# Kernel tuning notes

Measured on AMD Instinct MI355X. Metric: run time of the kernel, lower is better.

Reference implementation:

```python
import jax, jax.numpy as jnp
import numpy as np

D, NH, NL, NP, DFF = 256, 8, 4, 4, 1024
DH = D // NH
# 4-level FPN of a 1024x1024 image at strides 8/16/32/64 (H, W per level)
SHAPES = np.array([[128, 128], [64, 64], [32, 32], [16, 16]], dtype=np.int32)


def setup_inputs() -> dict:
    ks = jax.random.split(jax.random.key(0), 16)
    B, Lq = 4, 900
    sizes = SHAPES[:, 0] * SHAPES[:, 1]
    Lin = int(sizes.sum())
    starts = np.concatenate([[0], np.cumsum(sizes)[:-1]]).astype(np.int32)
    s = 0.02  # small init so softmax/LN stay well-conditioned

    def w(k, shape):
        return jax.random.normal(k, shape, jnp.float32) * s

    return {
        "tgt": jax.random.normal(ks[0], (Lq, B, D), jnp.float32),
        "tgt_reference_points": jax.random.uniform(ks[1], (Lq, B, NL, 2), jnp.float32),
        "memory": jax.random.normal(ks[2], (Lin, B, D), jnp.float32),
        "W_off": w(ks[3], (NH * NL * NP * 2, D)), "b_off": w(ks[4], (NH * NL * NP * 2,)),
        "W_attn": w(ks[5], (NH * NL * NP, D)), "b_attn": w(ks[6], (NH * NL * NP,)),
        "W_val": w(ks[7], (D, D)), "b_val": w(ks[8], (D,)),
        "W_out": w(ks[9], (D, D)), "b_out": w(ks[10], (D,)),
        "ln1_g": jnp.ones((D,), jnp.float32), "ln1_b": jnp.zeros((D,), jnp.float32),
        "W1": w(ks[11], (DFF, D)), "b1": w(ks[12], (DFF,)),
        "W2": w(ks[13], (D, DFF)), "b2": w(ks[14], (D,)),
        "ln3_g": jnp.ones((D,), jnp.float32), "ln3_b": jnp.zeros((D,), jnp.float32),
        "memory_spatial_shapes": jnp.asarray(SHAPES),
        "memory_level_start_index": jnp.asarray(starts),
        "memory_key_padding_mask": jnp.zeros((B, Lin), jnp.bool_),
    }


def _ln(x, g, b, eps=1e-5):
    mu = x.mean(-1, keepdims=True)
    var = ((x - mu) ** 2).mean(-1, keepdims=True)
    return (x - mu) * jax.lax.rsqrt(var + eps) * g + b


def _bilinear(vl, loc, H, W):
    # vl: (B, NH, H*W, DH); loc: (B, Lq, NH, NP, 2) normalized to [0,1]
    # matches torch grid_sample(mode='bilinear', padding_mode='zeros', align_corners=False)
    B, Lq, nh, P, _ = loc.shape
    x = loc[..., 0] * W - 0.5
    y = loc[..., 1] * H - 0.5
    x0f = jnp.floor(x)
    y0f = jnp.floor(y)
    x0 = x0f.astype(jnp.int32)
    y0 = y0f.astype(jnp.int32)
    wx1 = x - x0f
    wy1 = y - y0f

    def tap(xi, yi, w):
        valid = (xi >= 0) & (xi < W) & (yi >= 0) & (yi < H)
        idx = jnp.clip(yi, 0, H - 1) * W + jnp.clip(xi, 0, W - 1)
        idx = idx.transpose(0, 2, 1, 3).reshape(B, nh, Lq * P)
        ww = (w * valid).transpose(0, 2, 1, 3).reshape(B, nh, Lq * P)
        vals = jnp.take_along_axis(vl, idx[..., None], axis=2)  # (B,NH,Lq*P,DH)
        return vals * ww[..., None]

    acc = (tap(x0, y0, (1 - wx1) * (1 - wy1)) + tap(x0 + 1, y0, wx1 * (1 - wy1))
           + tap(x0, y0 + 1, (1 - wx1) * wy1) + tap(x0 + 1, y0 + 1, wx1 * wy1))
    return acc.reshape(B, nh, Lq, P, DH)


def _msda(q, ref, value, shapes_np, W_off, b_off, W_attn, b_attn, W_out, b_out):
    # q: (B,Lq,D), ref: (B,Lq,NL,2), value: (B,Lin,NH,DH)
    B, Lq, _ = q.shape
    off = (q @ W_off.T + b_off).reshape(B, Lq, NH, NL, NP, 2)
    a = jax.nn.softmax((q @ W_attn.T + b_attn).reshape(B, Lq, NH, NL * NP), axis=-1)
    a = a.reshape(B, Lq, NH, NL, NP)
    norm = jnp.asarray(shapes_np[:, ::-1].copy(), jnp.float32)  # (NL, 2) as (W, H)
    loc = ref[:, :, None, :, None, :] + off / norm[None, None, None, :, None, :]
    sizes = [int(h) * int(w) for h, w in shapes_np]
    starts = np.concatenate([[0], np.cumsum(sizes)[:-1]])
    v = value.transpose(0, 2, 1, 3)  # (B, NH, Lin, DH)
    out = jnp.zeros((B, NH, Lq, DH), q.dtype)
    for l, (H, W) in enumerate(shapes_np):
        vl = v[:, :, int(starts[l]):int(starts[l]) + sizes[l], :]
        sampled = _bilinear(vl, loc[:, :, :, l], int(H), int(W))  # (B,NH,Lq,NP,DH)
        wl = a[:, :, :, l].transpose(0, 2, 1, 3)  # (B,NH,Lq,NP)
        out = out + (sampled * wl[..., None]).sum(3)
    out = out.transpose(0, 2, 1, 3).reshape(B, Lq, D)
    return out @ W_out.T + b_out


def reference(tgt, tgt_reference_points, memory, W_off, b_off, W_attn, b_attn,
              W_val, b_val, W_out, b_out, ln1_g, ln1_b, W1, b1, W2, b2, ln3_g, ln3_b,
              memory_spatial_shapes, memory_level_start_index, memory_key_padding_mask):
    shapes_np = np.asarray(memory_spatial_shapes)  # static level metadata
    q = tgt.transpose(1, 0, 2)                      # (B, Lq, D)
    ref = tgt_reference_points.transpose(1, 0, 2, 3)
    mem = memory.transpose(1, 0, 2)                 # (B, Lin, D)
    B, Lin, _ = mem.shape
    value = mem @ W_val.T + b_val
    value = jnp.where(memory_key_padding_mask[..., None], 0.0, value)
    value = value.reshape(B, Lin, NH, DH)
    ca = _msda(q, ref, value, shapes_np, W_off, b_off, W_attn, b_attn, W_out, b_out)
    # residual + LN (dropout is identity in eval)
    t = _ln(tgt + ca.transpose(1, 0, 2), ln1_g, ln1_b)
    # FFN
    t2 = jax.nn.relu(t @ W1.T + b1) @ W2.T + b2
    return _ln(t + t2, ln3_g, ln3_b)
```

## Files before the change

### kernel.cpp

```cpp
#include <hip/hip_runtime.h>
#include <hip/hip_bf16.h>

#define B_   4
#define LQ_  900
#define D_   256
#define NH_  8
#define DH_  32
#define NL_  4
#define NP_  4
#define DFF_ 1024
#define LIN_ 21760
#define MQ_  (LQ_*B_)
#define MV_  (LIN_*B_)

typedef __attribute__((ext_vector_type(8))) short bh8;
typedef __attribute__((ext_vector_type(4))) float f32x4;

__device__ __forceinline__ short bf16b(float f) {
    __hip_bfloat16 h = __float2bfloat16(f);
    return *reinterpret_cast<short*>(&h);
}

__device__ __forceinline__ void gload_lds16(const void* g, void* l) {
    __builtin_amdgcn_global_load_lds(
        (const __attribute__((address_space(1))) unsigned int*)g,
        (__attribute__((address_space(3))) unsigned int*)l, 16, 0, 0);
}

__device__ __forceinline__ bh8 af_from_f32(const float* p) {
    float4 v0 = *reinterpret_cast<const float4*>(p);
    float4 v1 = *reinterpret_cast<const float4*>(p + 4);
    return (bh8){ bf16b(v0.x), bf16b(v0.y), bf16b(v0.z), bf16b(v0.w),
                  bf16b(v1.x), bf16b(v1.y), bf16b(v1.z), bf16b(v1.w) };
}

__global__ __launch_bounds__(256)
void wprep_k(const float* __restrict__ Woff, const float* __restrict__ Wattn,
             const float* __restrict__ Wout, const float* __restrict__ W1,
             const float* __restrict__ W2, const float* __restrict__ Wval,
             unsigned char* __restrict__ qkvimg, unsigned char* __restrict__ outimg,
             unsigned char* __restrict__ w1img, unsigned char* __restrict__ w2img,
             unsigned char* __restrict__ valimg)
{
    const int cid = blockIdx.x*256 + threadIdx.x;
    const float* W; unsigned char* img; int KQ, c;
    if      (cid < 8192)  { W=Woff;  img=qkvimg;           KQ=8;  c=cid;       }
    else if (cid < 12288) { W=Wattn; img=qkvimg + 131072;  KQ=8;  c=cid-8192;  }
    else if (cid < 20480) { W=Wout;  img=outimg;           KQ=8;  c=cid-12288; }
    else if (cid < 53248) { W=W1;    img=w1img;            KQ=8;  c=cid-20480; }
    else if (cid < 86016) { W=W2;    img=w2img;            KQ=32; c=cid-53248; }
    else                  { W=Wval;  img=valimg;           KQ=8;  c=cid-86016; }
    const int K   = KQ*32;
    const int n16 = c & 15, g = (c>>4)&3, t = c>>6;
    const int kq  = t & (KQ-1);
    const int ntile = t >> ((KQ==8) ? 3 : 5);
    const int n = ntile*16 + n16, k0 = kq*32 + g*8;
    float4 v0 = *reinterpret_cast<const float4*>(&W[(size_t)n*K + k0]);
    float4 v1 = *reinterpret_cast<const float4*>(&W[(size_t)n*K + k0 + 4]);
    union { short s[8]; uint4 u; } pk;
    pk.s[0]=bf16b(v0.x); pk.s[1]=bf16b(v0.y); pk.s[2]=bf16b(v0.z); pk.s[3]=bf16b(v0.w);
    pk.s[4]=bf16b(v1.x); pk.s[5]=bf16b(v1.y); pk.s[6]=bf16b(v1.z); pk.s[7]=bf16b(v1.w);
    *reinterpret_cast<uint4*>(img + (size_t)(ntile*KQ + kq)*1024 + (g*16+n16)*16) = pk.u;
}

__global__ __launch_bounds__(256, 4)
void val_gemm_k(const float* __restrict__ A, const unsigned char* __restrict__ Wimg,
                const float* __restrict__ bias, unsigned short* __restrict__ C,
                const unsigned char* __restrict__ mask)
{
    __shared__ __align__(16) unsigned char Al[32768];

    const int tid  = threadIdx.x;
    const int lane = tid & 63;
    const int wc   = tid >> 6;
    const int m0   = blockIdx.x * 32;
    const int r16  = lane & 15;
    const int g    = lane >> 4;

    const unsigned char* Abyte = (const unsigned char*)A;
    const unsigned char* wlane = Wimg + lane*16;

    const int a_row = (tid >> 3) & 31;
    const int a_x   = (tid & 7) * 16;
    const size_t a_src_row = (size_t)(m0 + a_row) * 1024 + (a_x ^ ((a_row & 7) << 4));
    const int a_dst = tid * 16;

#define ISSUE_A(KQ) gload_lds16(Abyte + a_src_row + (KQ)*128, (char*)Al + (KQ)*4096 + a_dst)
#define ISSUE_W(KQ, SLOT)                                                              \
    do { _Pragma("unroll")                                                             \
        for (int i_ = 0; i_ < 4; ++i_)                                                 \
            bfr[SLOT][i_] = *reinterpret_cast<const bh8*>(                             \
                wlane + (size_t)((wc*4 + i_)*8 + (KQ))*1024);                          \
    } while (0)

    bh8 bfr[3][4];

    ISSUE_A(0);
    ISSUE_W(0, 0);
    ISSUE_W(1, 1);
    ISSUE_A(1);
    ISSUE_A(2);

    f32x4 acc[2][4];
    #pragma unroll
    for (int i = 0; i < 2; ++i)
        #pragma unroll
        for (int j = 0; j < 4; ++j) acc[i][j] = (f32x4){0.f,0.f,0.f,0.f};

    #pragma unroll
    for (int kq = 0; kq < 8; ++kq) {
        if (kq < 6)      asm volatile("s_waitcnt vmcnt(6)" ::: "memory");
        else if (kq == 6) asm volatile("s_waitcnt vmcnt(5)" ::: "memory");
        else              asm volatile("s_waitcnt vmcnt(0)" ::: "memory");
        __builtin_amdgcn_s_barrier();

        bh8 af[2];
        #pragma unroll
        for (int mf = 0; mf < 2; ++mf) {
            const int row = mf*16 + r16;
            const int swz = (row & 7) << 4;
            const char* base = (const char*)Al + kq*4096 + row*128;
            float4 v0 = *reinterpret_cast<const float4*>(base + ((g*32     ) ^ swz));
            float4 v1 = *reinterpret_cast<const float4*>(base + ((g*32 + 16) ^ swz));
            af[mf] = (bh8){ bf16b(v0.x), bf16b(v0.y), bf16b(v0.z), bf16b(v0.w),
                            bf16b(v1.x), bf16b(v1.y), bf16b(v1.z), bf16b(v1.w) };
        }

        if (kq == 0) { ISSUE_W(2, 2); ISSUE_A(3); }
        if (kq == 1) { ISSUE_W(3, 0); ISSUE_A(4); }
        if (kq == 2) { ISSUE_W(4, 1); ISSUE_A(5); }
        if (kq == 3) { ISSUE_W(5, 2); ISSUE_A(6); }
        if (kq == 4) { ISSUE_W(6, 0); ISSUE_A(7); }
        if (kq == 5) { ISSUE_W(7, 1); }

        #pragma unroll
        for (int mf = 0; mf < 2; ++mf)
            #pragma unroll
            for (int i = 0; i < 4; ++i)
                acc[mf][i] = __builtin_amdgcn_mfma_f32_16x16x32_bf16(af[mf], bfr[kq % 3][i], acc[mf][i], 0, 0, 0);
    }
#undef ISSUE_A
#undef ISSUE_W

    float bv[4];
    #pragma unroll
    for (int i = 0; i < 4; ++i) bv[i] = bias[wc*64 + i*16 + r16];

    #pragma unroll
    for (int mf = 0; mf < 2; ++mf) {
        #pragma unroll
        for (int r = 0; r < 4; ++r) {
            const int gm = m0 + mf*16 + g*4 + r;
            const bool z = mask[(gm & 3)*LIN_ + (gm >> 2)] != 0;
            #pragma unroll
            for (int i = 0; i < 4; ++i) {
                float v = acc[mf][i][r] + bv[i];
                if (z) v = 0.f;
                C[(size_t)gm*256 + wc*64 + i*16 + r16] = (unsigned short)bf16b(v);
            }
        }
    }
}

__global__ __launch_bounds__(512)
void qkv_k(const float* __restrict__ A, const unsigned char* __restrict__ Wimg,
           const float* __restrict__ b_off, const float* __restrict__ b_attn,
           float* __restrict__ Yoff, float* __restrict__ Yattn)
{
    const int tid = threadIdx.x, lane = tid & 63, w = tid >> 6;
    const int m16 = lane & 15, g = lane >> 4;
    const int m0 = blockIdx.x * 16;

    bh8 af[8];
    #pragma unroll
    for (int kq = 0; kq < 8; ++kq)
        af[kq] = af_from_f32(&A[(size_t)(m0 + m16)*256 + kq*32 + g*8]);

    f32x4 acc[3];
    #pragma unroll
    for (int i = 0; i < 3; ++i) acc[i] = (f32x4){0.f,0.f,0.f,0.f};

    #pragma unroll
    for (int i = 0; i < 3; ++i) {
        const int nt = w*3 + i;
        #pragma unroll
        for (int kq = 0; kq < 8; ++kq) {
            bh8 bf = *reinterpret_cast<const bh8*>(Wimg + (size_t)(nt*8 + kq)*1024 + lane*16);
            acc[i] = __builtin_amdgcn_mfma_f32_16x16x32_bf16(af[kq], bf, acc[i], 0, 0, 0);
        }
    }

    #pragma unroll
    for (int i = 0; i < 3; ++i) {
        const int nt = w*3 + i;
        const int j  = nt*16 + m16;
        #pragma unroll
        for (int r = 0; r < 4; ++r) {
            const int m = m0 + g*4 + r;
            if (nt < 16) Yoff[(size_t)m*256 + j] = acc[i][r] + b_off[j];
            else         Yattn[(size_t)m*128 + (j-256)] = acc[i][r] + b_attn[j-256];
        }
    }
}

__global__ __launch_bounds__(1024, 4)
void outln_k(const float* __restrict__ A, const unsigned char* __restrict__ Wimg,
             const float* __restrict__ bias, const float* __restrict__ res,
             const float* __restrict__ lg, const float* __restrict__ lb,
             float* __restrict__ T)
{
    __shared__ float sln[16][256];

    const int tid = threadIdx.x, lane = tid & 63, w = tid >> 6;
    const int m16 = lane & 15, g = lane >> 4;
    const int m0 = blockIdx.x * 16;

    bh8 af[8];
    #pragma unroll
    for (int kq = 0; kq < 8; ++kq)
        af[kq] = af_from_f32(&A[(size_t)(m0 + m16)*256 + kq*32 + g*8]);

    f32x4 acc = (f32x4){0.f,0.f,0.f,0.f};
    #pragma unroll
    for (int kq = 0; kq < 8; ++kq) {
        bh8 bf = *reinterpret_cast<const bh8*>(Wimg + (size_t)(w*8 + kq)*1024 + lane*16);
        acc = __builtin_amdgcn_mfma_f32_16x16x32_bf16(af[kq], bf, acc, 0, 0, 0);
    }

    const int j = w*16 + m16;
    #pragma unroll
    for (int r = 0; r < 4; ++r) {
        const int ml = g*4 + r;
        sln[ml][j] = acc[r] + bias[j] + res[(size_t)(m0 + ml)*256 + j];
    }
    __syncthreads();

    const int row = tid >> 6, l2 = tid & 63;
    float v[4], s1 = 0.f, s2 = 0.f;
    #pragma unroll
    for (int c = 0; c < 4; ++c) {
        v[c] = sln[row][l2 + c*64];
        s1 += v[c]; s2 += v[c]*v[c];
    }
    #pragma unroll
    for (int o = 32; o >= 1; o >>= 1) {
        s1 += __shfl_xor(s1, o, 64);
        s2 += __shfl_xor(s2, o, 64);
    }
    const float mu  = s1 * (1.f/256.f);
    const float var = s2 * (1.f/256.f) - mu*mu;
    const float is  = rsqrtf(var + 1e-5f);
    #pragma unroll
    for (int c = 0; c < 4; ++c) {
        const int jj = l2 + c*64;
        T[(size_t)(m0 + row)*256 + jj] = (v[c] - mu) * is * lg[jj] + lb[jj];
    }
}

__global__ __launch_bounds__(1024, 4)
void ffnln_k(const float* __restrict__ T, const unsigned char* __restrict__ W1img,
             const float* __restrict__ b1, const unsigned char* __restrict__ W2img,
             const float* __restrict__ b2, const float* __restrict__ lg,
             const float* __restrict__ lb, float* __restrict__ Yout)
{
    __shared__ __align__(16) short hl[2][16*272];
    __shared__ float sln[16][256];

    const int tid = threadIdx.x, lane = tid & 63, w = tid >> 6;
    const int m16 = lane & 15, g = lane >> 4;
    const int m0 = blockIdx.x * 16;

    bh8 af1[8];
    #pragma unroll
    for (int kq = 0; kq < 8; ++kq)
        af1[kq] = af_from_f32(&T[(size_t)(m0 + m16)*256 + kq*32 + g*8]);

    f32x4 yacc = (f32x4){0.f,0.f,0.f,0.f};

    int buf = 0;
    #pragma unroll
    for (int fc = 0; fc < 4; ++fc) {
        const int ftile_g = fc*16 + w;
        f32x4 hacc = (f32x4){0.f,0.f,0.f,0.f};
        #pragma unroll
        for (int kq = 0; kq < 8; ++kq) {
            bh8 bf = *reinterpret_cast<const bh8*>(W1img + (size_t)(ftile_g*8 + kq)*1024 + lane*16);
            hacc = __builtin_amdgcn_mfma_f32_16x16x32_bf16(af1[kq], bf, hacc, 0, 0, 0);
        }
        const float bb = b1[ftile_g*16 + m16];
        #pragma unroll
        for (int r = 0; r < 4; ++r) {
            const float v = fmaxf(hacc[r] + bb, 0.f);
            hl[buf][(g*4 + r)*272 + w*16 + m16] = bf16b(v);
        }
        __syncthreads();
        bh8 a2[8];
        #pragma unroll
        for (int kqf = 0; kqf < 8; ++kqf)
            a2[kqf] = *reinterpret_cast<const bh8*>((const char*)&hl[buf][0]
                + m16*544 + (kqf*32 + g*8)*2);
        #pragma unroll
        for (int kqf = 0; kqf < 8; ++kqf) {
            const int kq2 = fc*8 + kqf;
            bh8 bf = *reinterpret_cast<const bh8*>(W2img + (size_t)(w*32 + kq2)*1024 + lane*16);
            yacc = __builtin_amdgcn_mfma_f32_16x16x32_bf16(a2[kqf], bf, yacc, 0, 0, 0);
        }
        buf ^= 1;
    }

    const int j = w*16 + m16;
    #pragma unroll
    for (int r = 0; r < 4; ++r) {
        const int ml = g*4 + r;
        sln[ml][j] = yacc[r] + b2[j] + T[(size_t)(m0 + ml)*256 + j];
    }
    __syncthreads();

    const int row = tid >> 6, l2 = tid & 63;
    float v[4], s1 = 0.f, s2 = 0.f;
    #pragma unroll
    for (int c = 0; c < 4; ++c) {
        v[c] = sln[row][l2 + c*64];
        s1 += v[c]; s2 += v[c]*v[c];
    }
    #pragma unroll
    for (int o = 32; o >= 1; o >>= 1) {
        s1 += __shfl_xor(s1, o, 64);
        s2 += __shfl_xor(s2, o, 64);
    }
    const float mu  = s1 * (1.f/256.f);
    const float var = s2 * (1.f/256.f) - mu*mu;
    const float is  = rsqrtf(var + 1e-5f);
    #pragma unroll
    for (int c = 0; c < 4; ++c) {
        const int jj = l2 + c*64;
        Yout[(size_t)(m0 + row)*256 + jj] = (v[c] - mu) * is * lg[jj] + lb[jj];
    }
}

__global__ __launch_bounds__(256)
void msda_k(const float* __restrict__ off,
            const float* __restrict__ attnlog,
            const float* __restrict__ refp,
            const __hip_bfloat16* __restrict__ value,
            float* __restrict__ out)
{
    const int m = blockIdx.x;
    const int b = m & 3;
    const int d = threadIdx.x;
    const int h = d >> 5;

    __shared__ float s_off[256];
    __shared__ float s_al[128];
    __shared__ float s_ref[NL_*2];
    s_off[d] = off[(size_t)m*256 + d];
    if (d < 128) s_al[d] = attnlog[(size_t)m*128 + d];
    if (d < NL_*2) s_ref[d] = refp[(size_t)m*(NL_*2) + d];
    __syncthreads();

    float mx = -1e30f;
    #pragma unroll
    for (int t = 0; t < 16; ++t) mx = fmaxf(mx, s_al[h*16 + t]);
    float e[16], ssum = 0.f;
    #pragma unroll
    for (int t = 0; t < 16; ++t) { e[t] = __expf(s_al[h*16 + t] - mx); ssum += e[t]; }
    const float inv = 1.f / ssum;

    const int HS[4] = {128, 64, 32, 16};
    const int ST[4] = {0, 16384, 20480, 21504};

    float acc = 0.f;
    #pragma unroll
    for (int l = 0; l < NL_; ++l) {
        const int H = HS[l], W = HS[l], st = ST[l];
        const float rx = s_ref[l*2+0], ry = s_ref[l*2+1];
        #pragma unroll
        for (int p = 0; p < NP_; ++p) {
            const int base = ((h*NL_ + l)*NP_ + p);
            const float a  = e[l*4 + p] * inv;
            const float ox = s_off[base*2+0], oy = s_off[base*2+1];
            const float x = rx*(float)W + ox - 0.5f;
            const float y = ry*(float)H + oy - 0.5f;
            const float x0f = floorf(x), y0f = floorf(y);
            const int x0 = (int)x0f, y0 = (int)y0f;
            const float wx1 = x - x0f, wy1 = y - y0f;
            const float wx0 = 1.f - wx1, wy0 = 1.f - wy1;
            #pragma unroll
            for (int t = 0; t < 4; ++t) {
                const int xi = x0 + (t & 1);
                const int yi = y0 + (t >> 1);
                const float wgt = (t==0 ? wx0*wy0 : t==1 ? wx1*wy0 : t==2 ? wx0*wy1 : wx1*wy1);
                if (xi >= 0 && xi < W && yi >= 0 && yi < H) {
                    const size_t idx = (size_t)(st + yi*W + xi);
                    const float v = __bfloat162float(value[(idx*B_ + b)*D_ + d]);
                    acc = fmaf(a*wgt, v, acc);
                }
            }
        }
    }
    out[(size_t)m*256 + d] = acc;
}

extern "C" void kernel_launch(void* const* d_in, const int* in_sizes, int n_in,
                              void* d_out, int out_size, void* d_ws, size_t ws_size,
                              hipStream_t stream)
{
    const float* tgt    = (const float*)d_in[0];
    const float* refp   = (const float*)d_in[1];
    const float* mem    = (const float*)d_in[2];
    const float* W_off  = (const float*)d_in[3];
    const float* b_off  = (const float*)d_in[4];
    const float* W_attn = (const float*)d_in[5];
    const float* b_attn = (const float*)d_in[6];
    const float* W_val  = (const float*)d_in[7];
    const float* b_val  = (const float*)d_in[8];
    const float* W_out  = (const float*)d_in[9];
    const float* b_out  = (const float*)d_in[10];
    const float* ln1g   = (const float*)d_in[11];
    const float* ln1b   = (const float*)d_in[12];
    const float* W1     = (const float*)d_in[13];
    const float* b1     = (const float*)d_in[14];
    const float* W2     = (const float*)d_in[15];
    const float* b2     = (const float*)d_in[16];
    const float* ln3g   = (const float*)d_in[17];
    const float* ln3b   = (const float*)d_in[18];
    const unsigned char* mask = (const unsigned char*)d_in[21];
    float* out = (float*)d_out;

    char* p = (char*)d_ws;
    __hip_bfloat16* value = (__hip_bfloat16*)p; p += (size_t)MV_*D_*2;
    float* offb = (float*)p; p += (size_t)MQ_*256*4;
    float* attl = (float*)p; p += (size_t)MQ_*128*4;
    float* msda = (float*)p; p += (size_t)MQ_*256*4;
    float* tb   = (float*)p; p += (size_t)MQ_*256*4;
    unsigned char* qkvimg = (unsigned char*)p; p += 196608;
    unsigned char* outimg = (unsigned char*)p; p += 131072;
    unsigned char* w1img  = (unsigned char*)p; p += 524288;
    unsigned char* w2img  = (unsigned char*)p; p += 524288;
    unsigned char* valimg = (unsigned char*)p; p += 131072;
    (void)ws_size; (void)in_sizes; (void)n_in; (void)out_size;

    wprep_k<<<dim3(368), dim3(256), 0, stream>>>(W_off, W_attn, W_out, W1, W2, W_val,
                                                 qkvimg, outimg, w1img, w2img, valimg);
    val_gemm_k<<<dim3(MV_/32), dim3(256), 0, stream>>>(mem, valimg, b_val,
                                                       (unsigned short*)value, mask);
    qkv_k<<<dim3(MQ_/16), dim3(512), 0, stream>>>(tgt, qkvimg, b_off, b_attn, offb, attl);
    msda_k<<<dim3(MQ_), dim3(256), 0, stream>>>(offb, attl, refp, value, msda);
    outln_k<<<dim3(MQ_/16), dim3(1024), 0, stream>>>(msda, outimg, b_out, tgt, ln1g, ln1b, tb);
    ffnln_k<<<dim3(MQ_/16), dim3(1024), 0, stream>>>(tb, w1img, b1, w2img, b2, ln3g, ln3b, out);
}
```

Before: 118.2 us.

## Split value GEMM N across two blocks with a 4-slot LDS ring

The value-projection GEMM now launches twice as many blocks, each computing half of the 256 output columns for a 32-row tile. The A-tile LDS staging drops from 8 slots to a 4-slot ring, halving shared memory, and the launch bound rises to 8 blocks per CU. The 3-deep register prefetch of B fragments is replaced by per-iteration loads of fewer fragments. The aim is more occupancy and parallelism, at the cost of reading each fp32 A tile twice (relying on L2) and exposing B-load latency directly.

```diff
diff --git a/kernel.cpp b/kernel.cpp
--- a/kernel.cpp
+++ b/kernel.cpp
@@ -63,19 +63,21 @@
     *reinterpret_cast<uint4*>(img + (size_t)(ntile*KQ + kq)*1024 + (g*16+n16)*16) = pk.u;
 }
 
-__global__ __launch_bounds__(256, 4)
+__global__ __launch_bounds__(256, 8)
 void val_gemm_k(const float* __restrict__ A, const unsigned char* __restrict__ Wimg,
                 const float* __restrict__ bias, unsigned short* __restrict__ C,
                 const unsigned char* __restrict__ mask)
 {
-    __shared__ __align__(16) unsigned char Al[32768];
-
-    const int tid  = threadIdx.x;
-    const int lane = tid & 63;
-    const int wc   = tid >> 6;
-    const int m0   = blockIdx.x * 32;
-    const int r16  = lane & 15;
-    const int g    = lane >> 4;
+    __shared__ __align__(16) unsigned char Al[16384];
+
+    const int tid   = threadIdx.x;
+    const int lane  = tid & 63;
+    const int wc    = tid >> 6;
+    const int mt    = blockIdx.x >> 1;
+    const int nhalf = blockIdx.x & 1;
+    const int m0    = mt * 32;
+    const int r16   = lane & 15;
+    const int g     = lane >> 4;
 
     const unsigned char* Abyte = (const unsigned char*)A;
     const unsigned char* wlane = Wimg + lane*16;
@@ -85,32 +87,22 @@
     const size_t a_src_row = (size_t)(m0 + a_row) * 1024 + (a_x ^ ((a_row & 7) << 4));
     const int a_dst = tid * 16;
 
-#define ISSUE_A(KQ) gload_lds16(Abyte + a_src_row + (KQ)*128, (char*)Al + (KQ)*4096 + a_dst)
-#define ISSUE_W(KQ, SLOT)                                                              \
-    do { _Pragma("unroll")                                                             \
-        for (int i_ = 0; i_ < 4; ++i_)                                                 \
-            bfr[SLOT][i_] = *reinterpret_cast<const bh8*>(                             \
-                wlane + (size_t)((wc*4 + i_)*8 + (KQ))*1024);                          \
-    } while (0)
-
-    bh8 bfr[3][4];
+#define ISSUE_A(KQ) gload_lds16(Abyte + a_src_row + (KQ)*128, (char*)Al + ((KQ)&3)*4096 + a_dst)
 
     ISSUE_A(0);
-    ISSUE_W(0, 0);
-    ISSUE_W(1, 1);
     ISSUE_A(1);
     ISSUE_A(2);
 
-    f32x4 acc[2][4];
+    f32x4 acc[2][2];
     #pragma unroll
     for (int i = 0; i < 2; ++i)
         #pragma unroll
-        for (int j = 0; j < 4; ++j) acc[i][j] = (f32x4){0.f,0.f,0.f,0.f};
+        for (int j = 0; j < 2; ++j) acc[i][j] = (f32x4){0.f,0.f,0.f,0.f};
 
     #pragma unroll
     for (int kq = 0; kq < 8; ++kq) {
-        if (kq < 6)      asm volatile("s_waitcnt vmcnt(6)" ::: "memory");
-        else if (kq == 6) asm volatile("s_waitcnt vmcnt(5)" ::: "memory");
+        if (kq < 6)      asm volatile("s_waitcnt vmcnt(2)" ::: "memory");
+        else if (kq == 6) asm volatile("s_waitcnt vmcnt(1)" ::: "memory");
         else              asm volatile("s_waitcnt vmcnt(0)" ::: "memory");
         __builtin_amdgcn_s_barrier();
 
@@ -119,32 +111,29 @@
         for (int mf = 0; mf < 2; ++mf) {
             const int row = mf*16 + r16;
             const int swz = (row & 7) << 4;
-            const char* base = (const char*)Al + kq*4096 + row*128;
+            const char* base = (const char*)Al + (kq & 3)*4096 + row*128;
             float4 v0 = *reinterpret_cast<const float4*>(base + ((g*32     ) ^ swz));
             float4 v1 = *reinterpret_cast<const float4*>(base + ((g*32 + 16) ^ swz));
             af[mf] = (bh8){ bf16b(v0.x), bf16b(v0.y), bf16b(v0.z), bf16b(v0.w),
                             bf16b(v1.x), bf16b(v1.y), bf16b(v1.z), bf16b(v1.w) };
         }
 
-        if (kq == 0) { ISSUE_W(2, 2); ISSUE_A(3); }
-        if (kq == 1) { ISSUE_W(3, 0); ISSUE_A(4); }
-        if (kq == 2) { ISSUE_W(4, 1); ISSUE_A(5); }
-        if (kq == 3) { ISSUE_W(5, 2); ISSUE_A(6); }
-        if (kq == 4) { ISSUE_W(6, 0); ISSUE_A(7); }
-        if (kq == 5) { ISSUE_W(7, 1); }
-
-        #pragma unroll
-        for (int mf = 0; mf < 2; ++mf)
+        if (kq < 5) ISSUE_A(kq + 3);
+
+        #pragma unroll
+        for (int i = 0; i < 2; ++i) {
+            const int nt = nhalf*8 + wc*2 + i;
+            bh8 bf = *reinterpret_cast<const bh8*>(wlane + (size_t)(nt*8 + kq)*1024);
             #pragma unroll
-            for (int i = 0; i < 4; ++i)
-                acc[mf][i] = __builtin_amdgcn_mfma_f32_16x16x32_bf16(af[mf], bfr[kq % 3][i], acc[mf][i], 0, 0, 0);
+            for (int mf = 0; mf < 2; ++mf)
+                acc[mf][i] = __builtin_amdgcn_mfma_f32_16x16x32_bf16(af[mf], bf, acc[mf][i], 0, 0, 0);
+        }
     }
 #undef ISSUE_A
-#undef ISSUE_W
-
-    float bv[4];
-    #pragma unroll
-    for (int i = 0; i < 4; ++i) bv[i] = bias[wc*64 + i*16 + r16];
+
+    float bv[2];
+    #pragma unroll
+    for (int i = 0; i < 2; ++i) bv[i] = bias[nhalf*128 + wc*32 + i*16 + r16];
 
     #pragma unroll
     for (int mf = 0; mf < 2; ++mf) {
@@ -153,10 +142,10 @@
             const int gm = m0 + mf*16 + g*4 + r;
             const bool z = mask[(gm & 3)*LIN_ + (gm >> 2)] != 0;
             #pragma unroll
-            for (int i = 0; i < 4; ++i) {
+            for (int i = 0; i < 2; ++i) {
                 float v = acc[mf][i][r] + bv[i];
                 if (z) v = 0.f;
-                C[(size_t)gm*256 + wc*64 + i*16 + r16] = (unsigned short)bf16b(v);
+                C[(size_t)gm*256 + nhalf*128 + wc*32 + i*16 + r16] = (unsigned short)bf16b(v);
             }
         }
     }
@@ -442,8 +431,8 @@
 
     wprep_k<<<dim3(368), dim3(256), 0, stream>>>(W_off, W_attn, W_out, W1, W2, W_val,
                                                  qkvimg, outimg, w1img, w2img, valimg);
-    val_gemm_k<<<dim3(MV_/32), dim3(256), 0, stream>>>(mem, valimg, b_val,
-                                                       (unsigned short*)value, mask);
+    val_gemm_k<<<dim3((MV_/32)*2), dim3(256), 0, stream>>>(mem, valimg, b_val,
+                                                           (unsigned short*)value, mask);
     qkv_k<<<dim3(MQ_/16), dim3(512), 0, stream>>>(tgt, qkvimg, b_off, b_attn, offb, attl);
     msda_k<<<dim3(MQ_), dim3(256), 0, stream>>>(offb, attl, refp, value, msda);
     outln_k<<<dim3(MQ_/16), dim3(1024), 0, stream>>>(msda, outimg, b_out, tgt, ln1g, ln1b, tb);
```

Result: slower. 126.2 us (+6.8%).

## Fuse value and offset/attn projection GEMMs; fuse out-proj LN with FFN LN

Applied to the files above, without the earlier changes.

Merges the value projection GEMM and the query offset/attention projection into one launch, with the query blocks appended after the value blocks. The query part now uses 256-thread blocks, so each wave computes 6 N-tiles instead of 3. It also fuses the output projection, residual and first LayerNorm into the FFN kernel, keeping the normalized rows in shared memory. This removes the intermediate tb buffer round-trip and two kernel launches. The cost is lower occupancy on the fused FFN kernel (launch bounds 1024,2) and more register pressure in the qkv branch.

```diff
diff --git a/kernel.cpp b/kernel.cpp
--- a/kernel.cpp
+++ b/kernel.cpp
@@ -12,6 +12,7 @@
 #define LIN_ 21760
 #define MQ_  (LQ_*B_)
 #define MV_  (LIN_*B_)
+#define VALBLKS (MV_/32)
 
 typedef __attribute__((ext_vector_type(8))) short bh8;
 typedef __attribute__((ext_vector_type(4))) float f32x4;
@@ -64,26 +65,31 @@
 }
 
 __global__ __launch_bounds__(256, 4)
-void val_gemm_k(const float* __restrict__ A, const unsigned char* __restrict__ Wimg,
-                const float* __restrict__ bias, unsigned short* __restrict__ C,
-                const unsigned char* __restrict__ mask)
+void valqkv_k(const float* __restrict__ A, const unsigned char* __restrict__ Wimg,
+              const float* __restrict__ bias, unsigned short* __restrict__ C,
+              const unsigned char* __restrict__ mask,
+              const float* __restrict__ tgt, const unsigned char* __restrict__ Qimg,
+              const float* __restrict__ b_off, const float* __restrict__ b_attn,
+              float* __restrict__ Yoff, float* __restrict__ Yattn)
 {
     __shared__ __align__(16) unsigned char Al[32768];
 
     const int tid  = threadIdx.x;
     const int lane = tid & 63;
-    const int wc   = tid >> 6;
-    const int m0   = blockIdx.x * 32;
-    const int r16  = lane & 15;
-    const int g    = lane >> 4;
-
-    const unsigned char* Abyte = (const unsigned char*)A;
-    const unsigned char* wlane = Wimg + lane*16;
-
-    const int a_row = (tid >> 3) & 31;
-    const int a_x   = (tid & 7) * 16;
-    const size_t a_src_row = (size_t)(m0 + a_row) * 1024 + (a_x ^ ((a_row & 7) << 4));
-    const int a_dst = tid * 16;
+
+    if (blockIdx.x < VALBLKS) {
+        const int wc   = tid >> 6;
+        const int m0   = blockIdx.x * 32;
+        const int r16  = lane & 15;
+        const int g    = lane >> 4;
+
+        const unsigned char* Abyte = (const unsigned char*)A;
+        const unsigned char* wlane = Wimg + lane*16;
+
+        const int a_row = (tid >> 3) & 31;
+        const int a_x   = (tid & 7) * 16;
+        const size_t a_src_row = (size_t)(m0 + a_row) * 1024 + (a_x ^ ((a_row & 7) << 4));
+        const int a_dst = tid * 16;
 
 #define ISSUE_A(KQ) gload_lds16(Abyte + a_src_row + (KQ)*128, (char*)Al + (KQ)*4096 + a_dst)
 #define ISSUE_W(KQ, SLOT)                                                              \
@@ -93,187 +99,177 @@
                 wlane + (size_t)((wc*4 + i_)*8 + (KQ))*1024);                          \
     } while (0)
 
-    bh8 bfr[3][4];
-
-    ISSUE_A(0);
-    ISSUE_W(0, 0);
-    ISSUE_W(1, 1);
-    ISSUE_A(1);
-    ISSUE_A(2);
-
-    f32x4 acc[2][4];
-    #pragma unroll
-    for (int i = 0; i < 2; ++i)
-        #pragma unroll
-        for (int j = 0; j < 4; ++j) acc[i][j] = (f32x4){0.f,0.f,0.f,0.f};
-
-    #pragma unroll
-    for (int kq = 0; kq < 8; ++kq) {
-        if (kq < 6)      asm volatile("s_waitcnt vmcnt(6)" ::: "memory");
-        else if (kq == 6) asm volatile("s_waitcnt vmcnt(5)" ::: "memory");
-        else              asm volatile("s_waitcnt vmcnt(0)" ::: "memory");
-        __builtin_amdgcn_s_barrier();
-
-        bh8 af[2];
-        #pragma unroll
-        for (int mf = 0; mf < 2; ++mf) {
-            const int row = mf*16 + r16;
-            const int swz = (row & 7) << 4;
-            const char* base = (const char*)Al + kq*4096 + row*128;
-            float4 v0 = *reinterpret_cast<const float4*>(base + ((g*32     ) ^ swz));
-            float4 v1 = *reinterpret_cast<const float4*>(base + ((g*32 + 16) ^ swz));
-            af[mf] = (bh8){ bf16b(v0.x), bf16b(v0.y), bf16b(v0.z), bf16b(v0.w),
-                            bf16b(v1.x), bf16b(v1.y), bf16b(v1.z), bf16b(v1.w) };
-        }
-
-        if (kq == 0) { ISSUE_W(2, 2); ISSUE_A(3); }
-        if (kq == 1) { ISSUE_W(3, 0); ISSUE_A(4); }
-        if (kq == 2) { ISSUE_W(4, 1); ISSUE_A(5); }
-        if (kq == 3) { ISSUE_W(5, 2); ISSUE_A(6); }
-        if (kq == 4) { ISSUE_W(6, 0); ISSUE_A(7); }
-        if (kq == 5) { ISSUE_W(7, 1); }
-
-        #pragma unroll
-        for (int mf = 0; mf < 2; ++mf)
-            #pragma unroll
-            for (int i = 0; i < 4; ++i)
-                acc[mf][i] = __builtin_amdgcn_mfma_f32_16x16x32_bf16(af[mf], bfr[kq % 3][i], acc[mf][i], 0, 0, 0);
-    }
+        bh8 bfr[3][4];
+
+        ISSUE_A(0);
+        ISSUE_W(0, 0);
+        ISSUE_W(1, 1);
+        ISSUE_A(1);
+        ISSUE_A(2);
+
+        f32x4 acc[2][4];
+        #pragma unroll
+        for (int i = 0; i < 2; ++i)
+            #pragma unroll
+            for (int j = 0; j < 4; ++j) acc[i][j] = (f32x4){0.f,0.f,0.f,0.f};
+
+        #pragma unroll
+        for (int kq = 0; kq < 8; ++kq) {
+            if (kq < 6)      asm volatile("s_waitcnt vmcnt(6)" ::: "memory");
+            else if (kq == 6) asm volatile("s_waitcnt vmcnt(5)" ::: "memory");
+            else              asm volatile("s_waitcnt vmcnt(0)" ::: "memory");
+            __builtin_amdgcn_s_barrier();
+
+            bh8 af[2];
+            #pragma unroll
+            for (int mf = 0; mf < 2; ++mf) {
+                const int row = mf*16 + r16;
+                const int swz = (row & 7) << 4;
+                const char* base = (const char*)Al + kq*4096 + row*128;
+                float4 v0 = *reinterpret_cast<const float4*>(base + ((g*32     ) ^ swz));
+                float4 v1 = *reinterpret_cast<const float4*>(base + ((g*32 + 16) ^ swz));
+                af[mf] = (bh8){ bf16b(v0.x), bf16b(v0.y), bf16b(v0.z), bf16b(v0.w),
+                                bf16b(v1.x), bf16b(v1.y), bf16b(v1.z), bf16b(v1.w) };
+            }
+
+            if (kq == 0) { ISSUE_W(2, 2); ISSUE_A(3); }
+            if (kq == 1) { ISSUE_W(3, 0); ISSUE_A(4); }
+            if (kq == 2) { ISSUE_W(4, 1); ISSUE_A(5); }
+            if (kq == 3) { ISSUE_W(5, 2); ISSUE_A(6); }
+            if (kq == 4) { ISSUE_W(6, 0); ISSUE_A(7); }
+            if (kq == 5) { ISSUE_W(7, 1); }
+
+            #pragma unroll
+            for (int mf = 0; mf < 2; ++mf)
+                #pragma unroll
+                for (int i = 0; i < 4; ++i)
+                    acc[mf][i] = __builtin_amdgcn_mfma_f32_16x16x32_bf16(af[mf], bfr[kq % 3][i], acc[mf][i], 0, 0, 0);
+        }
 #undef ISSUE_A
 #undef ISSUE_W
 
-    float bv[4];
-    #pragma unroll
-    for (int i = 0; i < 4; ++i) bv[i] = bias[wc*64 + i*16 + r16];
-
-    #pragma unroll
-    for (int mf = 0; mf < 2; ++mf) {
-        #pragma unroll
-        for (int r = 0; r < 4; ++r) {
-            const int gm = m0 + mf*16 + g*4 + r;
-            const bool z = mask[(gm & 3)*LIN_ + (gm >> 2)] != 0;
-            #pragma unroll
-            for (int i = 0; i < 4; ++i) {
-                float v = acc[mf][i][r] + bv[i];
-                if (z) v = 0.f;
-                C[(size_t)gm*256 + wc*64 + i*16 + r16] = (unsigned short)bf16b(v);
+        float bv[4];
+        #pragma unroll
+        for (int i = 0; i < 4; ++i) bv[i] = bias[wc*64 + i*16 + r16];
+
+        #pragma unroll
+        for (int mf = 0; mf < 2; ++mf) {
+            #pragma unroll
+            for (int r = 0; r < 4; ++r) {
+                const int gm = m0 + mf*16 + g*4 + r;
+                const bool z = mask[(gm & 3)*LIN_ + (gm >> 2)] != 0;
+                #pragma unroll
+                for (int i = 0; i < 4; ++i) {
+                    float v = acc[mf][i][r] + bv[i];
+                    if (z) v = 0.f;
+                    C[(size_t)gm*256 + wc*64 + i*16 + r16] = (unsigned short)bf16b(v);
+                }
             }
         }
-    }
-}
-
-__global__ __launch_bounds__(512)
-void qkv_k(const float* __restrict__ A, const unsigned char* __restrict__ Wimg,
-           const float* __restrict__ b_off, const float* __restrict__ b_attn,
-           float* __restrict__ Yoff, float* __restrict__ Yattn)
+    } else {
+        const int w   = tid >> 6;
+        const int m16 = lane & 15, g = lane >> 4;
+        const int m0  = (blockIdx.x - VALBLKS) * 16;
+
+        bh8 af[8];
+        #pragma unroll
+        for (int kq = 0; kq < 8; ++kq)
+            af[kq] = af_from_f32(&tgt[(size_t)(m0 + m16)*256 + kq*32 + g*8]);
+
+        f32x4 acc[6];
+        #pragma unroll
+        for (int i = 0; i < 6; ++i) acc[i] = (f32x4){0.f,0.f,0.f,0.f};
+
+        #pragma unroll
+        for (int i = 0; i < 6; ++i) {
+            const int nt = w*6 + i;
+            #pragma unroll
+            for (int kq = 0; kq < 8; ++kq) {
+                bh8 bf = *reinterpret_cast<const bh8*>(Qimg + (size_t)(nt*8 + kq)*1024 + lane*16);
+                acc[i] = __builtin_amdgcn_mfma_f32_16x16x32_bf16(af[kq], bf, acc[i], 0, 0, 0);
+            }
+        }
+
+        #pragma unroll
+        for (int i = 0; i < 6; ++i) {
+            const int nt = w*6 + i;
+            const int j  = nt*16 + m16;
+            #pragma unroll
+            for (int r = 0; r < 4; ++r) {
+                const int m = m0 + g*4 + r;
+                if (nt < 16) Yoff[(size_t)m*256 + j] = acc[i][r] + b_off[j];
+                else         Yattn[(size_t)m*128 + (j-256)] = acc[i][r] + b_attn[j-256];
+            }
+        }
+    }
+}
+
+__global__ __launch_bounds__(1024, 2)
+void outffn_k(const float* __restrict__ Amsda, const unsigned char* __restrict__ Oimg,
+              const float* __restrict__ b_out, const float* __restrict__ res,
+              const float* __restrict__ l1g, const float* __restrict__ l1b,
+              const unsigned char* __restrict__ W1img, const float* __restrict__ b1,
+              const unsigned char* __restrict__ W2img, const float* __restrict__ b2,
+              const float* __restrict__ l3g, const float* __restrict__ l3b,
+              float* __restrict__ Yout)
 {
+    __shared__ float sln[16][256];
+    __shared__ __align__(16) short hl[2][16*272];
+
     const int tid = threadIdx.x, lane = tid & 63, w = tid >> 6;
     const int m16 = lane & 15, g = lane >> 4;
     const int m0 = blockIdx.x * 16;
 
-    bh8 af[8];
-    #pragma unroll
-    for (int kq = 0; kq < 8; ++kq)
-        af[kq] = af_from_f32(&A[(size_t)(m0 + m16)*256 + kq*32 + g*8]);
-
-    f32x4 acc[3];
-    #pragma unroll
-    for (int i = 0; i < 3; ++i) acc[i] = (f32x4){0.f,0.f,0.f,0.f};
-
-    #pragma unroll
-    for (int i = 0; i < 3; ++i) {
-        const int nt = w*3 + i;
+    {
+        bh8 af[8];
+        #pragma unroll
+        for (int kq = 0; kq < 8; ++kq)
+            af[kq] = af_from_f32(&Amsda[(size_t)(m0 + m16)*256 + kq*32 + g*8]);
+
+        f32x4 acc = (f32x4){0.f,0.f,0.f,0.f};
         #pragma unroll
         for (int kq = 0; kq < 8; ++kq) {
-            bh8 bf = *reinterpret_cast<const bh8*>(Wimg + (size_t)(nt*8 + kq)*1024 + lane*16);
-            acc[i] = __builtin_amdgcn_mfma_f32_16x16x32_bf16(af[kq], bf, acc[i], 0, 0, 0);
-        }
-    }
-
-    #pragma unroll
-    for (int i = 0; i < 3; ++i) {
-        const int nt = w*3 + i;
-        const int j  = nt*16 + m16;
+            bh8 bf = *reinterpret_cast<const bh8*>(Oimg + (size_t)(w*8 + kq)*1024 + lane*16);
+            acc = __builtin_amdgcn_mfma_f32_16x16x32_bf16(af[kq], bf, acc, 0, 0, 0);
+        }
+
+        const int j = w*16 + m16;
         #pragma unroll
         for (int r = 0; r < 4; ++r) {
-            const int m = m0 + g*4 + r;
-            if (nt < 16) Yoff[(size_t)m*256 + j] = acc[i][r] + b_off[j];
-            else         Yattn[(size_t)m*128 + (j-256)] = acc[i][r] + b_attn[j-256];
-        }
-    }
-}
-
-__global__ __launch_bounds__(1024, 4)
-void outln_k(const float* __restrict__ A, const unsigned char* __restrict__ Wimg,
-             const float* __restrict__ bias, const float* __restrict__ res,
-             const float* __restrict__ lg, const float* __restrict__ lb,
-             float* __restrict__ T)
-{
-    __shared__ float sln[16][256];
-
-    const int tid = threadIdx.x, lane = tid & 63, w = tid >> 6;
-    const int m16 = lane & 15, g = lane >> 4;
-    const int m0 = blockIdx.x * 16;
-
-    bh8 af[8];
-    #pragma unroll
-    for (int kq = 0; kq < 8; ++kq)
-        af[kq] = af_from_f32(&A[(size_t)(m0 + m16)*256 + kq*32 + g*8]);
-
-    f32x4 acc = (f32x4){0.f,0.f,0.f,0.f};
-    #pragma unroll
-    for (int kq = 0; kq < 8; ++kq) {
-        bh8 bf = *reinterpret_cast<const bh8*>(Wimg + (size_t)(w*8 + kq)*1024 + lane*16);
-        acc = __builtin_amdgcn_mfma_f32_16x16x32_bf16(af[kq], bf, acc, 0, 0, 0);
-    }
-
-    const int j = w*16 + m16;
-    #pragma unroll
-    for (int r = 0; r < 4; ++r) {
-        const int ml = g*4 + r;
-        sln[ml][j] = acc[r] + bias[j] + res[(size_t)(m0 + ml)*256 + j];
+            const int ml = g*4 + r;
+            sln[ml][j] = acc[r] + b_out[j] + res[(size_t)(m0 + ml)*256 + j];
+        }
     }
     __syncthreads();
 
-    const int row = tid >> 6, l2 = tid & 63;
-    float v[4], s1 = 0.f, s2 = 0.f;
-    #pragma unroll
-    for (int c = 0; c < 4; ++c) {
-        v[c] = sln[row][l2 + c*64];
-        s1 += v[c]; s2 += v[c]*v[c];
-    }
-    #pragma unroll
-    for (int o = 32; o >= 1; o >>= 1) {
-        s1 += __shfl_xor(s1, o, 64);
-        s2 += __shfl_xor(s2, o, 64);
-    }
-    const float mu  = s1 * (1.f/256.f);
-    const float var = s2 * (1.f/256.f) - mu*mu;
-    const float is  = rsqrtf(var + 1e-5f);
-    #pragma unroll
-    for (int c = 0; c < 4; ++c) {
-        const int jj = l2 + c*64;
-        T[(size_t)(m0 + row)*256 + jj] = (v[c] - mu) * is * lg[jj] + lb[jj];
-    }
-}
-
-__global__ __launch_bounds__(1024, 4)
-void ffnln_k(const float* __restrict__ T, const unsigned char* __restrict__ W1img,
-             const float* __restrict__ b1, const unsigned char* __restrict__ W2img,
-             const float* __restrict__ b2, const float* __restrict__ lg,
-             const float* __restrict__ lb, float* __restrict__ Yout)
-{
-    __shared__ __align__(16) short hl[2][16*272];
-    __shared__ float sln[16][256];
-
-    const int tid = threadIdx.x, lane = tid & 63, w = tid >> 6;
-    const int m16 = lane & 15, g = lane >> 4;
-    const int m0 = blockIdx.x * 16;
+    {
+        const int row = w, l2 = lane;
+        float v[4], s1 = 0.f, s2 = 0.f;
+        #pragma unroll
+        for (int c = 0; c < 4; ++c) {
+            v[c] = sln[row][l2 + c*64];
+            s1 += v[c]; s2 += v[c]*v[c];
+        }
+        #pragma unroll
+        for (int o = 32; o >= 1; o >>= 1) {
+            s1 += __shfl_xor(s1, o, 64);
+            s2 += __shfl_xor(s2, o, 64);
+        }
+        const float mu  = s1 * (1.f/256.f);
+        const float var = s2 * (1.f/256.f) - mu*mu;
+        const float is  = rsqrtf(var + 1e-5f);
+        #pragma unroll
+        for (int c = 0; c < 4; ++c) {
+            const int jj = l2 + c*64;
+            sln[row][jj] = (v[c] - mu) * is * l1g[jj] + l1b[jj];
+        }
+    }
+    __syncthreads();
 
     bh8 af1[8];
     #pragma unroll
     for (int kq = 0; kq < 8; ++kq)
-        af1[kq] = af_from_f32(&T[(size_t)(m0 + m16)*256 + kq*32 + g*8]);
+        af1[kq] = af_from_f32(&sln[m16][kq*32 + g*8]);
 
     f32x4 yacc = (f32x4){0.f,0.f,0.f,0.f};
 
@@ -308,33 +304,37 @@
         buf ^= 1;
     }
 
-    const int j = w*16 + m16;
-    #pragma unroll
-    for (int r = 0; r < 4; ++r) {
-        const int ml = g*4 + r;
-        sln[ml][j] = yacc[r] + b2[j] + T[(size_t)(m0 + ml)*256 + j];
+    {
+        const int j = w*16 + m16;
+        #pragma unroll
+        for (int r = 0; r < 4; ++r) {
+            const int ml = g*4 + r;
+            sln[ml][j] = yacc[r] + b2[j] + sln[ml][j];
+        }
     }
     __syncthreads();
 
-    const int row = tid >> 6, l2 = tid & 63;
-    float v[4], s1 = 0.f, s2 = 0.f;
-    #pragma unroll
-    for (int c = 0; c < 4; ++c) {
-        v[c] = sln[row][l2 + c*64];
-        s1 += v[c]; s2 += v[c]*v[c];
-    }
-    #pragma unroll
-    for (int o = 32; o >= 1; o >>= 1) {
-        s1 += __shfl_xor(s1, o, 64);
-        s2 += __shfl_xor(s2, o, 64);
-    }
-    const float mu  = s1 * (1.f/256.f);
-    const float var = s2 * (1.f/256.f) - mu*mu;
-    const float is  = rsqrtf(var + 1e-5f);
-    #pragma unroll
-    for (int c = 0; c < 4; ++c) {
-        const int jj = l2 + c*64;
-        Yout[(size_t)(m0 + row)*256 + jj] = (v[c] - mu) * is * lg[jj] + lb[jj];
+    {
+        const int row = w, l2 = lane;
+        float v[4], s1 = 0.f, s2 = 0.f;
+        #pragma unroll
+        for (int c = 0; c < 4; ++c) {
+            v[c] = sln[row][l2 + c*64];
+            s1 += v[c]; s2 += v[c]*v[c];
+        }
+        #pragma unroll
+        for (int o = 32; o >= 1; o >>= 1) {
+            s1 += __shfl_xor(s1, o, 64);
+            s2 += __shfl_xor(s2, o, 64);
+        }
+        const float mu  = s1 * (1.f/256.f);
+        const float var = s2 * (1.f/256.f) - mu*mu;
+        const float is  = rsqrtf(var + 1e-5f);
+        #pragma unroll
+        for (int c = 0; c < 4; ++c) {
+            const int jj = l2 + c*64;
+            Yout[(size_t)(m0 + row)*256 + jj] = (v[c] - mu) * is * l3g[jj] + l3b[jj];
+        }
     }
 }
 
@@ -432,7 +432,6 @@
     float* offb = (float*)p; p += (size_t)MQ_*256*4;
     float* attl = (float*)p; p += (size_t)MQ_*128*4;
     float* msda = (float*)p; p += (size_t)MQ_*256*4;
-    float* tb   = (float*)p; p += (size_t)MQ_*256*4;
     unsigned char* qkvimg = (unsigned char*)p; p += 196608;
     unsigned char* outimg = (unsigned char*)p; p += 131072;
     unsigned char* w1img  = (unsigned char*)p; p += 524288;
@@ -442,10 +441,11 @@
 
     wprep_k<<<dim3(368), dim3(256), 0, stream>>>(W_off, W_attn, W_out, W1, W2, W_val,
                                                  qkvimg, outimg, w1img, w2img, valimg);
-    val_gemm_k<<<dim3(MV_/32), dim3(256), 0, stream>>>(mem, valimg, b_val,
-                                                       (unsigned short*)value, mask);
-    qkv_k<<<dim3(MQ_/16), dim3(512), 0, stream>>>(tgt, qkvimg, b_off, b_attn, offb, attl);
+    valqkv_k<<<dim3(VALBLKS + MQ_/16), dim3(256), 0, stream>>>(
+        mem, valimg, b_val, (unsigned short*)value, mask,
+        tgt, qkvimg, b_off, b_attn, offb, attl);
     msda_k<<<dim3(MQ_), dim3(256), 0, stream>>>(offb, attl, refp, value, msda);
-    outln_k<<<dim3(MQ_/16), dim3(1024), 0, stream>>>(msda, outimg, b_out, tgt, ln1g, ln1b, tb);
-    ffnln_k<<<dim3(MQ_/16), dim3(1024), 0, stream>>>(tb, w1img, b1, w2img, b2, ln3g, ln3b, out);
-}
+    outffn_k<<<dim3(MQ_/16), dim3(1024), 0, stream>>>(
+        msda, outimg, b_out, tgt, ln1g, ln1b,
+        w1img, b1, w2img, b2, ln3g, ln3b, out);
+}
```

Result: faster. 115.7 us (-2.1%).
